# Kernel tuning notes

Measured on AMD Instinct MI355X. Metric: run time of the kernel, lower is better.

## Reference

```python
import jax, jax.numpy as jnp
import numpy as np

N_ENT = 100000
K = 64
D = 500            # emb_dim (complex half-dim); entity embedding is 2*D
R = 237            # num_relations
ATTN = 128
B = 1024
ETA_MAX = 0.5


def setup_inputs() -> dict:
    key = jax.random.key(0)
    ks = jax.random.split(key, 12)
    anchor_ids = jax.random.randint(ks[0], (B,), 0, N_ENT)
    nbr_ent = jax.random.randint(ks[1], (N_ENT, K), 0, N_ENT)
    nbr_rel = jax.random.randint(ks[2], (N_ENT, K), 0, R)
    nbr_dir = jax.random.randint(ks[3], (N_ENT, K), 0, 2).astype(bool)
    nbr_mask = jax.random.randint(ks[4], (N_ENT, K), 0, 2).astype(bool)
    freq = jax.random.uniform(ks[5], (N_ENT,), dtype=jnp.float32) * 1000.0
    entity_embedding = jax.random.normal(ks[6], (N_ENT, 2 * D), dtype=jnp.float32) * 0.1
    # relation phases; get_relation_reim -> (cos(phase), sin(phase))
    rel_phase = jax.random.uniform(ks[7], (R, D), dtype=jnp.float32, minval=-np.pi, maxval=np.pi)
    a_param = jnp.ones((D,), dtype=jnp.float32)
    eta_raw = jnp.float32(-6.0)
    w_raw = jnp.float32(1.0)
    b = jnp.float32(0.0)
    Wq = jax.random.normal(ks[8], (ATTN, 2 * D), dtype=jnp.float32) * 0.01
    Wk = jax.random.normal(ks[9], (ATTN, 2 * D), dtype=jnp.float32) * 0.01
    rel_bias = jax.random.normal(ks[10], (R, 1), dtype=jnp.float32) * 0.01
    dir_bias = jax.random.normal(ks[11], (2, 1), dtype=jnp.float32) * 0.01
    return dict(anchor_ids=anchor_ids, nbr_ent=nbr_ent, nbr_rel=nbr_rel,
                nbr_dir=nbr_dir, nbr_mask=nbr_mask, freq=freq,
                entity_embedding=entity_embedding, rel_phase=rel_phase,
                a_param=a_param, eta_raw=eta_raw, w_raw=w_raw, b=b,
                Wq=Wq, Wk=Wk, rel_bias=rel_bias, dir_bias=dir_bias)


def reference(anchor_ids, nbr_ent, nbr_rel, nbr_dir, nbr_mask, freq,
              entity_embedding, rel_phase, a_param, eta_raw, w_raw, b,
              Wq, Wk, rel_bias, dir_bias):
    # gather per-anchor neighbor tables: [B, K]
    a_ent = nbr_ent[anchor_ids]
    a_rel = nbr_rel[anchor_ids]
    a_dir = nbr_dir[anchor_ids]
    a_msk = nbr_mask[anchor_ids]

    # neighbor entity embeddings [B, K, 2D] -> complex halves [B, K, D]
    e_j = entity_embedding[a_ent]
    re_j, im_j = jnp.split(e_j, 2, axis=-1)

    # RotatE relation rotation (conjugate when dir==True)
    phase = rel_phase[a_rel]                      # [B, K, D]
    re_r = jnp.cos(phase)
    im_r = jnp.sin(phase)
    im_sel = jnp.where(a_dir[..., None], -im_r, im_r)
    re_msg = re_j * re_r - im_j * im_sel
    im_msg = re_j * im_sel + im_j * re_r
    hat = jnp.concatenate([re_msg, im_msg], axis=-1)  # [B, K, 2D]

    e_i = entity_embedding[anchor_ids]            # [B, 2D]

    # small QK attention with relation/direction bias
    q = e_i @ Wq.T                                # [B, A]
    k = hat @ Wk.T                                # [B, K, A]
    scale = max(ATTN ** 0.5, 1e-6)
    logits = jnp.einsum('ba,bka->bk', q, k) / scale
    dir_id = a_dir.astype(jnp.int32)
    logits = logits + rel_bias[a_rel][..., 0] + dir_bias[dir_id][..., 0]
    logits = jnp.where(a_msk, logits, -10000.0)

    has_nbr = jnp.any(a_msk, axis=1)              # [B]
    logits = jnp.where(has_nbr[:, None], logits, 0.0)
    attn = jax.nn.softmax(logits, axis=1)
    attn = jnp.where(has_nbr[:, None], attn, 0.0)

    delta = jnp.einsum('bk,bkd->bd', attn, hat)   # [B, 2D]
    delta = jnp.where(has_nbr[:, None], delta, e_i)

    # frequency-gated interpolation
    logf = jnp.log1p(freq[anchor_ids])
    w = jax.nn.softplus(w_raw)
    eta = ETA_MAX * jax.nn.sigmoid(eta_raw + w * (-logf) + b)
    eta = eta * has_nbr.astype(eta.dtype)

    re_d, im_d = jnp.split(delta, 2, axis=-1)
    re_d = a_param * re_d
    im_d = a_param * im_d
    re_i, im_i = jnp.split(e_i, 2, axis=-1)
    re_out = re_i + eta[:, None] * (re_d - re_i)
    im_out = im_i + eta[:, None] * (im_d - im_i)
    return jnp.concatenate([re_out, im_out], axis=-1)
```

## Files before the change

kernel.cpp:

```cpp
#include <hip/hip_runtime.h>
#include <math.h>

#define N_ENT 100000
#define KNBR 64
#define DHALF 500
#define TWO_D 1000
#define ATTN_DIM 128
#define ETA_MAX 0.5f

__global__ __launch_bounds__(256) void precompute_m(
    const int* __restrict__ anchor_ids,
    const float* __restrict__ E,
    const float* __restrict__ Wq,
    const float* __restrict__ Wk,
    float* __restrict__ M, int B)
{
    __shared__ float e_lds[8][TWO_D];
    __shared__ float qp[2][8][ATTN_DIM];
    __shared__ float q_lds[8][ATTN_DIM];
    const int t  = threadIdx.x;
    const int b0 = blockIdx.x * 8;

    for (int j = 0; j < 8; ++j) {
        int bb = b0 + j;
        int row = (bb < B) ? anchor_ids[bb] : 0;
        if (t < 250) {
            const float4* src = (const float4*)(E + (size_t)row * TWO_D);
            float4 v = src[t];
            e_lds[j][4 * t + 0] = v.x;
            e_lds[j][4 * t + 1] = v.y;
            e_lds[j][4 * t + 2] = v.z;
            e_lds[j][4 * t + 3] = v.w;
        }
    }
    __syncthreads();

    {
        const int a = t & 127;
        const int h = t >> 7;
        float acc[8] = {0.f, 0.f, 0.f, 0.f, 0.f, 0.f, 0.f, 0.f};
        const float* wrow = Wq + (size_t)a * TWO_D + h * DHALF;
        for (int d = 0; d < DHALF; ++d) {
            float w = wrow[d];
            int dd = h * DHALF + d;
#pragma unroll
            for (int j = 0; j < 8; ++j) acc[j] += w * e_lds[j][dd];
        }
#pragma unroll
        for (int j = 0; j < 8; ++j) qp[h][j][a] = acc[j];
    }
    __syncthreads();
    for (int idx = t; idx < 8 * ATTN_DIM; idx += 256) {
        ((float*)q_lds)[idx] = ((float*)qp)[idx] + ((float*)qp)[8 * ATTN_DIM + idx];
    }
    __syncthreads();

    const float inv_scale = 0.0883883476483184f;
    float acc2[4][8];
#pragma unroll
    for (int c = 0; c < 4; ++c)
#pragma unroll
        for (int j = 0; j < 8; ++j) acc2[c][j] = 0.f;

    for (int a = 0; a < ATTN_DIM; ++a) {
        const float* wkrow = Wk + (size_t)a * TWO_D;
        float wk[4];
#pragma unroll
        for (int c = 0; c < 4; ++c) {
            int d = t + 256 * c;
            wk[c] = (d < TWO_D) ? wkrow[d] : 0.f;
        }
#pragma unroll
        for (int j = 0; j < 8; ++j) {
            float qv = q_lds[j][a];
#pragma unroll
            for (int c = 0; c < 4; ++c) acc2[c][j] += qv * wk[c];
        }
    }
#pragma unroll
    for (int c = 0; c < 4; ++c) {
        int d = t + 256 * c;
        if (d < TWO_D) {
#pragma unroll
            for (int j = 0; j < 8; ++j) {
                int bb = b0 + j;
                if (bb < B) M[(size_t)bb * TWO_D + d] = acc2[c][j] * inv_scale;
            }
        }
    }
}

__global__ __launch_bounds__(256) void refine(
    const int* __restrict__ anchor_ids,
    const int* __restrict__ nbr_ent,
    const int* __restrict__ nbr_rel,
    const int* __restrict__ nbr_dir,
    const int* __restrict__ nbr_mask,
    const float* __restrict__ freq,
    const float* __restrict__ E,
    const float* __restrict__ P,
    const float* __restrict__ a_param,
    const float* __restrict__ eta_raw_p,
    const float* __restrict__ w_raw_p,
    const float* __restrict__ b_p,
    const float* __restrict__ rel_bias,
    const float* __restrict__ dir_bias,
    const float* __restrict__ M,
    float* __restrict__ out)
{
    __shared__ float m_lds[TWO_D];
    __shared__ float accm[4][TWO_D];
    __shared__ float sum_s[4];
    __shared__ int ent_s[KNBR], rel_s[KNBR], dir_s[KNBR], msk_s[KNBR];

    const int t = threadIdx.x;
    const int bid = blockIdx.x;
    const int anchor = anchor_ids[bid];

    for (int idx = t; idx < TWO_D; idx += 256)
        m_lds[idx] = M[(size_t)bid * TWO_D + idx];
    if (t < KNBR) {
        size_t off = (size_t)anchor * KNBR + t;
        ent_s[t] = nbr_ent[off];
        rel_s[t] = nbr_rel[off];
        dir_s[t] = nbr_dir[off];
        msk_s[t] = nbr_mask[off];
    }
    __syncthreads();

    const int lane = t & 63;
    const int wid = t >> 6;

    float mre[8], mim[8];
#pragma unroll
    for (int i = 0; i < 8; ++i) {
        int d = lane + 64 * i;
        mre[i] = (d < DHALF) ? m_lds[d] : 0.f;
        mim[i] = (d < DHALF) ? m_lds[DHALF + d] : 0.f;
    }

    float accre[8], accim[8];
#pragma unroll
    for (int i = 0; i < 8; ++i) { accre[i] = 0.f; accim[i] = 0.f; }
    float wsum = 0.f;
    const float db0 = dir_bias[0];
    const float db1 = dir_bias[1];

    for (int k = wid; k < KNBR; k += 4) {
        if (!msk_s[k]) continue;
        const int ent = ent_s[k];
        const int rel = rel_s[k];
        const int dirf = dir_s[k];
        const float* erow = E + (size_t)ent * TWO_D;
        const float* prow = P + (size_t)rel * DHALF;

        float hre[8], him[8];
        float dot = 0.f;
#pragma unroll
        for (int i = 0; i < 8; ++i) {
            int d = lane + 64 * i;
            if (d < DHALF) {
                float re = erow[d];
                float im = erow[DHALF + d];
                float ph = prow[d];
                float s, c;
                __sincosf(ph, &s, &c);
                if (dirf) s = -s;
                hre[i] = re * c - im * s;
                him[i] = re * s + im * c;
                dot += mre[i] * hre[i] + mim[i] * him[i];
            } else {
                hre[i] = 0.f;
                him[i] = 0.f;
            }
        }
        dot += __shfl_xor(dot, 32);
        dot += __shfl_xor(dot, 16);
        dot += __shfl_xor(dot, 8);
        dot += __shfl_xor(dot, 4);
        dot += __shfl_xor(dot, 2);
        dot += __shfl_xor(dot, 1);

        float logit = dot + rel_bias[rel] + (dirf ? db1 : db0);
        float p = __expf(logit);
        wsum += p;
#pragma unroll
        for (int i = 0; i < 8; ++i) {
            accre[i] += p * hre[i];
            accim[i] += p * him[i];
        }
    }

    if (lane == 0) sum_s[wid] = wsum;
#pragma unroll
    for (int i = 0; i < 8; ++i) {
        int d = lane + 64 * i;
        if (d < DHALF) {
            accm[wid][d] = accre[i];
            accm[wid][DHALF + d] = accim[i];
        }
    }
    __syncthreads();

    const float S = sum_s[0] + sum_s[1] + sum_s[2] + sum_s[3];
    const float invS = (S > 0.f) ? 1.f / S : 0.f;
    float eta = 0.f;
    if (S > 0.f) {
        float logf_ = log1pf(freq[anchor]);
        float wv = log1pf(__expf(w_raw_p[0]));
        float x = eta_raw_p[0] - wv * logf_ + b_p[0];
        eta = ETA_MAX / (1.f + __expf(-x));
    }

    const float* eirow = E + (size_t)anchor * TWO_D;
#pragma unroll
    for (int c = 0; c < 4; ++c) {
        int dd = t + 256 * c;
        if (dd < TWO_D) {
            float delta = (accm[0][dd] + accm[1][dd] + accm[2][dd] + accm[3][dd]) * invS;
            float ei = eirow[dd];
            float ap = a_param[(dd < DHALF) ? dd : dd - DHALF];
            out[(size_t)bid * TWO_D + dd] = ei + eta * (ap * delta - ei);
        }
    }
}

extern "C" void kernel_launch(void* const* d_in, const int* in_sizes, int n_in,
                              void* d_out, int out_size, void* d_ws, size_t ws_size,
                              hipStream_t stream)
{
    const int*   anchor_ids = (const int*)d_in[0];
    const int*   nbr_ent    = (const int*)d_in[1];
    const int*   nbr_rel    = (const int*)d_in[2];
    const int*   nbr_dir    = (const int*)d_in[3];
    const int*   nbr_mask   = (const int*)d_in[4];
    const float* freq       = (const float*)d_in[5];
    const float* E          = (const float*)d_in[6];
    const float* P          = (const float*)d_in[7];
    const float* a_param    = (const float*)d_in[8];
    const float* eta_raw    = (const float*)d_in[9];
    const float* w_raw      = (const float*)d_in[10];
    const float* b_scalar   = (const float*)d_in[11];
    const float* Wq         = (const float*)d_in[12];
    const float* Wk         = (const float*)d_in[13];
    const float* rel_bias   = (const float*)d_in[14];
    const float* dir_bias   = (const float*)d_in[15];
    float* out = (float*)d_out;

    const int B = in_sizes[0];
    float* M = (float*)d_ws;

    precompute_m<<<(B + 7) / 8, 256, 0, stream>>>(anchor_ids, E, Wq, Wk, M, B);
    refine<<<B, 256, 0, stream>>>(anchor_ids, nbr_ent, nbr_rel, nbr_dir, nbr_mask,
                                  freq, E, P, a_param, eta_raw, w_raw, b_scalar,
                                  rel_bias, dir_bias, M, out);
}
```

Baseline: 629.1 us.

## Precompute Wq^T Wk, sincos tables, tiled M GEMM, and compacted prefetching neighbor loop

Replaces the per-anchor Q/K projection with a precomputed 1000x1000 matrix G2 = Wq^T Wk / scale, followed by a tiled GEMM from gathered anchor embeddings to M. Relation cos/sin values now come from tables built once per call instead of per-neighbor sincos. The refine kernel compacts masked neighbors with a ballot, folds the relation and direction biases in up front, and software-prefetches the next neighbor's float4 rows while computing the current one. In exchange it adds more kernel launches and a larger GEMM (1000x1000x128 plus 1024x1000x1000), which may cost more FLOPs than the original factored path.

```diff
diff --git a/kernel.cpp b/kernel.cpp
--- a/kernel.cpp
+++ b/kernel.cpp
@@ -1,93 +1,189 @@
 #include <hip/hip_runtime.h>
 #include <math.h>
 
-#define N_ENT 100000
 #define KNBR 64
 #define DHALF 500
 #define TWO_D 1000
 #define ATTN_DIM 128
 #define ETA_MAX 0.5f
 
-__global__ __launch_bounds__(256) void precompute_m(
-    const int* __restrict__ anchor_ids,
-    const float* __restrict__ E,
-    const float* __restrict__ Wq,
-    const float* __restrict__ Wk,
-    float* __restrict__ M, int B)
-{
-    __shared__ float e_lds[8][TWO_D];
-    __shared__ float qp[2][8][ATTN_DIM];
-    __shared__ float q_lds[8][ATTN_DIM];
-    const int t  = threadIdx.x;
-    const int b0 = blockIdx.x * 8;
-
-    for (int j = 0; j < 8; ++j) {
-        int bb = b0 + j;
-        int row = (bb < B) ? anchor_ids[bb] : 0;
-        if (t < 250) {
-            const float4* src = (const float4*)(E + (size_t)row * TWO_D);
-            float4 v = src[t];
-            e_lds[j][4 * t + 0] = v.x;
-            e_lds[j][4 * t + 1] = v.y;
-            e_lds[j][4 * t + 2] = v.z;
-            e_lds[j][4 * t + 3] = v.w;
-        }
+__global__ __launch_bounds__(256) void build_tables(
+    const float* __restrict__ P, float* __restrict__ ctab,
+    float* __restrict__ stab, int R)
+{
+    int idx = blockIdx.x * 256 + threadIdx.x;
+    if (idx >= R * 512) return;
+    int r = idx >> 9, d = idx & 511;
+    float c = 0.f, s = 0.f;
+    if (d < DHALF) { float ph = P[r * DHALF + d]; sincosf(ph, &s, &c); }
+    ctab[idx] = c;
+    stab[idx] = s;
+}
+
+__global__ __launch_bounds__(256) void build_g2(
+    const float* __restrict__ Wq, const float* __restrict__ Wk,
+    float* __restrict__ G2)
+{
+    __shared__ float At[ATTN_DIM][64];
+    __shared__ float Bt[ATTN_DIM][64];
+    const int t = threadIdx.x;
+    const int d1_0 = blockIdx.y * 64, d2_0 = blockIdx.x * 64;
+#pragma unroll
+    for (int i = 0; i < 32; ++i) {
+        int idx = t + 256 * i;
+        int a = idx >> 6, c = idx & 63;
+        int d1 = d1_0 + c, d2 = d2_0 + c;
+        At[a][c] = (d1 < TWO_D) ? Wq[(size_t)a * TWO_D + d1] : 0.f;
+        Bt[a][c] = (d2 < TWO_D) ? Wk[(size_t)a * TWO_D + d2] : 0.f;
     }
     __syncthreads();
-
-    {
-        const int a = t & 127;
-        const int h = t >> 7;
-        float acc[8] = {0.f, 0.f, 0.f, 0.f, 0.f, 0.f, 0.f, 0.f};
-        const float* wrow = Wq + (size_t)a * TWO_D + h * DHALF;
-        for (int d = 0; d < DHALF; ++d) {
-            float w = wrow[d];
-            int dd = h * DHALF + d;
-#pragma unroll
-            for (int j = 0; j < 8; ++j) acc[j] += w * e_lds[j][dd];
-        }
-#pragma unroll
-        for (int j = 0; j < 8; ++j) qp[h][j][a] = acc[j];
-    }
+    const int tx = t & 15, ty = t >> 4;
+    float acc[4][4] = {};
+    for (int a = 0; a < ATTN_DIM; ++a) {
+        float av[4], bv[4];
+#pragma unroll
+        for (int i = 0; i < 4; ++i) av[i] = At[a][4 * ty + i];
+#pragma unroll
+        for (int j = 0; j < 4; ++j) bv[j] = Bt[a][4 * tx + j];
+#pragma unroll
+        for (int i = 0; i < 4; ++i)
+#pragma unroll
+            for (int j = 0; j < 4; ++j) acc[i][j] += av[i] * bv[j];
+    }
+    const float inv_scale = 0.0883883476483184f;
+#pragma unroll
+    for (int i = 0; i < 4; ++i) {
+        int d1 = d1_0 + 4 * ty + i;
+        if (d1 < TWO_D) {
+#pragma unroll
+            for (int j = 0; j < 4; ++j) {
+                int d2 = d2_0 + 4 * tx + j;
+                G2[(size_t)d1 * 1024 + d2] = acc[i][j] * inv_scale;
+            }
+        }
+    }
+}
+
+__global__ __launch_bounds__(256) void gemm_M(
+    const int* __restrict__ anchor_ids, const float* __restrict__ E,
+    const float* __restrict__ G2, float* __restrict__ M, int B)
+{
+    __shared__ float At[64][33];
+    __shared__ float Bt[32][64];
+    __shared__ int rows_s[64];
+    const int t = threadIdx.x;
+    const int bx = blockIdx.x, by = blockIdx.y;
+    if (t < 64) { int bb = by * 64 + t; rows_s[t] = (bb < B) ? anchor_ids[bb] : 0; }
     __syncthreads();
-    for (int idx = t; idx < 8 * ATTN_DIM; idx += 256) {
-        ((float*)q_lds)[idx] = ((float*)qp)[idx] + ((float*)qp)[8 * ATTN_DIM + idx];
-    }
-    __syncthreads();
-
-    const float inv_scale = 0.0883883476483184f;
-    float acc2[4][8];
-#pragma unroll
-    for (int c = 0; c < 4; ++c)
-#pragma unroll
-        for (int j = 0; j < 8; ++j) acc2[c][j] = 0.f;
-
-    for (int a = 0; a < ATTN_DIM; ++a) {
-        const float* wkrow = Wk + (size_t)a * TWO_D;
-        float wk[4];
-#pragma unroll
-        for (int c = 0; c < 4; ++c) {
-            int d = t + 256 * c;
-            wk[c] = (d < TWO_D) ? wkrow[d] : 0.f;
-        }
-#pragma unroll
-        for (int j = 0; j < 8; ++j) {
-            float qv = q_lds[j][a];
-#pragma unroll
-            for (int c = 0; c < 4; ++c) acc2[c][j] += qv * wk[c];
-        }
-    }
-#pragma unroll
-    for (int c = 0; c < 4; ++c) {
-        int d = t + 256 * c;
-        if (d < TWO_D) {
-#pragma unroll
-            for (int j = 0; j < 8; ++j) {
-                int bb = b0 + j;
-                if (bb < B) M[(size_t)bb * TWO_D + d] = acc2[c][j] * inv_scale;
+    const int tx = t & 15, ty = t >> 4;
+    float acc[4][4] = {};
+    for (int k0 = 0; k0 < TWO_D; k0 += 32) {
+#pragma unroll
+        for (int i = 0; i < 8; ++i) {
+            int idx = t + 256 * i;
+            int r = idx >> 5, c = idx & 31;
+            int k = k0 + c;
+            At[r][c] = (k < TWO_D) ? E[(size_t)rows_s[r] * TWO_D + k] : 0.f;
+        }
+#pragma unroll
+        for (int i = 0; i < 8; ++i) {
+            int idx = t + 256 * i;
+            int r = idx >> 6, c = idx & 63;
+            int k = k0 + r;
+            Bt[r][c] = (k < TWO_D) ? G2[(size_t)k * 1024 + bx * 64 + c] : 0.f;
+        }
+        __syncthreads();
+#pragma unroll
+        for (int kk = 0; kk < 32; ++kk) {
+            float av[4], bv[4];
+#pragma unroll
+            for (int i = 0; i < 4; ++i) av[i] = At[4 * ty + i][kk];
+#pragma unroll
+            for (int j = 0; j < 4; ++j) bv[j] = Bt[kk][4 * tx + j];
+#pragma unroll
+            for (int i = 0; i < 4; ++i)
+#pragma unroll
+                for (int j = 0; j < 4; ++j) acc[i][j] += av[i] * bv[j];
+        }
+        __syncthreads();
+    }
+#pragma unroll
+    for (int i = 0; i < 4; ++i) {
+        int b = by * 64 + 4 * ty + i;
+        if (b < B) {
+#pragma unroll
+            for (int j = 0; j < 4; ++j) {
+                int d2 = bx * 64 + 4 * tx + j;
+                if (d2 < TWO_D) M[(size_t)b * TWO_D + d2] = acc[i][j];
             }
         }
     }
+}
+
+struct NbrData {
+    float4 re0, re1, im0, im1, c0, c1, s0, s1;
+    float rb, ds;
+};
+
+__device__ __forceinline__ void load_nbr(
+    int j, int lane, const float* __restrict__ E,
+    const float* __restrict__ ctab, const float* __restrict__ stab,
+    const int* ent_s, const int* rel_s, const float* rb_s, const float* ds_s,
+    NbrData& n)
+{
+    const int ent = ent_s[j];
+    const int rel = rel_s[j];
+    const float4* er = (const float4*)(E + (size_t)ent * TWO_D);
+    const float4* cr = (const float4*)(ctab + (size_t)rel * 512);
+    const float4* sr = (const float4*)(stab + (size_t)rel * 512);
+    n.re0 = er[lane];
+    n.im0 = er[125 + lane];
+    n.re1 = make_float4(0.f, 0.f, 0.f, 0.f);
+    n.im1 = make_float4(0.f, 0.f, 0.f, 0.f);
+    if (lane < 61) {
+        n.re1 = er[64 + lane];
+        n.im1 = er[189 + lane];
+    }
+    n.c0 = cr[lane];      n.c1 = cr[64 + lane];
+    n.s0 = sr[lane];      n.s1 = sr[64 + lane];
+    n.rb = rb_s[j];
+    n.ds = ds_s[j];
+}
+
+__device__ __forceinline__ void compute_nbr(
+    const NbrData& n,
+    const float4& mre0, const float4& mre1, const float4& mim0, const float4& mim1,
+    float4& are0, float4& are1, float4& aim0, float4& aim1, float& wsum)
+{
+    const float ds = n.ds;
+    float4 hre0, hre1, him0, him1;
+    float dot = 0.f;
+#define ROT_DOT(F)                                                              \
+    {                                                                           \
+        float se0 = n.s0.F * ds;                                                \
+        hre0.F = n.re0.F * n.c0.F - n.im0.F * se0;                              \
+        him0.F = n.re0.F * se0 + n.im0.F * n.c0.F;                              \
+        dot += mre0.F * hre0.F + mim0.F * him0.F;                               \
+        float se1 = n.s1.F * ds;                                                \
+        hre1.F = n.re1.F * n.c1.F - n.im1.F * se1;                              \
+        him1.F = n.re1.F * se1 + n.im1.F * n.c1.F;                              \
+        dot += mre1.F * hre1.F + mim1.F * him1.F;                               \
+    }
+    ROT_DOT(x) ROT_DOT(y) ROT_DOT(z) ROT_DOT(w)
+#undef ROT_DOT
+    dot += __shfl_xor(dot, 32);
+    dot += __shfl_xor(dot, 16);
+    dot += __shfl_xor(dot, 8);
+    dot += __shfl_xor(dot, 4);
+    dot += __shfl_xor(dot, 2);
+    dot += __shfl_xor(dot, 1);
+    const float p = __expf(dot + n.rb);
+    wsum += p;
+#define ACC(F)                                                                  \
+    are0.F += p * hre0.F; are1.F += p * hre1.F;                                 \
+    aim0.F += p * him0.F; aim1.F += p * him1.F;
+    ACC(x) ACC(y) ACC(z) ACC(w)
+#undef ACC
 }
 
 __global__ __launch_bounds__(256) void refine(
@@ -98,7 +194,8 @@
     const int* __restrict__ nbr_mask,
     const float* __restrict__ freq,
     const float* __restrict__ E,
-    const float* __restrict__ P,
+    const float* __restrict__ ctab,
+    const float* __restrict__ stab,
     const float* __restrict__ a_param,
     const float* __restrict__ eta_raw_p,
     const float* __restrict__ w_raw_p,
@@ -108,97 +205,66 @@
     const float* __restrict__ M,
     float* __restrict__ out)
 {
-    __shared__ float m_lds[TWO_D];
     __shared__ float accm[4][TWO_D];
     __shared__ float sum_s[4];
-    __shared__ int ent_s[KNBR], rel_s[KNBR], dir_s[KNBR], msk_s[KNBR];
+    __shared__ int ent_s[KNBR], rel_s[KNBR];
+    __shared__ float rb_s[KNBR], ds_s[KNBR];
+    __shared__ int act_n_s;
 
     const int t = threadIdx.x;
     const int bid = blockIdx.x;
-    const int anchor = anchor_ids[bid];
-
-    for (int idx = t; idx < TWO_D; idx += 256)
-        m_lds[idx] = M[(size_t)bid * TWO_D + idx];
-    if (t < KNBR) {
-        size_t off = (size_t)anchor * KNBR + t;
-        ent_s[t] = nbr_ent[off];
-        rel_s[t] = nbr_rel[off];
-        dir_s[t] = nbr_dir[off];
-        msk_s[t] = nbr_mask[off];
-    }
-    __syncthreads();
-
     const int lane = t & 63;
     const int wid = t >> 6;
-
-    float mre[8], mim[8];
-#pragma unroll
-    for (int i = 0; i < 8; ++i) {
-        int d = lane + 64 * i;
-        mre[i] = (d < DHALF) ? m_lds[d] : 0.f;
-        mim[i] = (d < DHALF) ? m_lds[DHALF + d] : 0.f;
-    }
-
-    float accre[8], accim[8];
-#pragma unroll
-    for (int i = 0; i < 8; ++i) { accre[i] = 0.f; accim[i] = 0.f; }
+    const int anchor = anchor_ids[bid];
+
+    if (wid == 0) {
+        size_t off = (size_t)anchor * KNBR + lane;
+        int msk = nbr_mask[off];
+        unsigned long long bal = __ballot(msk != 0);
+        if (msk) {
+            int rank = __popcll(bal & ((1ull << lane) - 1ull));
+            int rel = nbr_rel[off];
+            int dirf = nbr_dir[off];
+            ent_s[rank] = nbr_ent[off];
+            rel_s[rank] = rel;
+            ds_s[rank] = dirf ? -1.f : 1.f;
+            rb_s[rank] = rel_bias[rel] + dir_bias[dirf ? 1 : 0];
+        }
+        if (lane == 0) act_n_s = (int)__popcll(bal);
+    }
+    __syncthreads();
+    const int an = act_n_s;
+
+    const float4* mr = (const float4*)(M + (size_t)bid * TWO_D);
+    float4 mre0 = mr[lane];
+    float4 mim0 = mr[125 + lane];
+    float4 mre1 = make_float4(0.f, 0.f, 0.f, 0.f);
+    float4 mim1 = make_float4(0.f, 0.f, 0.f, 0.f);
+    if (lane < 61) { mre1 = mr[64 + lane]; mim1 = mr[189 + lane]; }
+
+    float4 are0 = make_float4(0.f, 0.f, 0.f, 0.f), are1 = are0, aim0 = are0, aim1 = are0;
     float wsum = 0.f;
-    const float db0 = dir_bias[0];
-    const float db1 = dir_bias[1];
-
-    for (int k = wid; k < KNBR; k += 4) {
-        if (!msk_s[k]) continue;
-        const int ent = ent_s[k];
-        const int rel = rel_s[k];
-        const int dirf = dir_s[k];
-        const float* erow = E + (size_t)ent * TWO_D;
-        const float* prow = P + (size_t)rel * DHALF;
-
-        float hre[8], him[8];
-        float dot = 0.f;
-#pragma unroll
-        for (int i = 0; i < 8; ++i) {
-            int d = lane + 64 * i;
-            if (d < DHALF) {
-                float re = erow[d];
-                float im = erow[DHALF + d];
-                float ph = prow[d];
-                float s, c;
-                __sincosf(ph, &s, &c);
-                if (dirf) s = -s;
-                hre[i] = re * c - im * s;
-                him[i] = re * s + im * c;
-                dot += mre[i] * hre[i] + mim[i] * him[i];
-            } else {
-                hre[i] = 0.f;
-                him[i] = 0.f;
-            }
-        }
-        dot += __shfl_xor(dot, 32);
-        dot += __shfl_xor(dot, 16);
-        dot += __shfl_xor(dot, 8);
-        dot += __shfl_xor(dot, 4);
-        dot += __shfl_xor(dot, 2);
-        dot += __shfl_xor(dot, 1);
-
-        float logit = dot + rel_bias[rel] + (dirf ? db1 : db0);
-        float p = __expf(logit);
-        wsum += p;
-#pragma unroll
-        for (int i = 0; i < 8; ++i) {
-            accre[i] += p * hre[i];
-            accim[i] += p * him[i];
-        }
+
+    NbrData cur, nxt;
+    int j = wid;
+    bool have = (j < an);
+    if (have) load_nbr(j, lane, E, ctab, stab, ent_s, rel_s, rb_s, ds_s, cur);
+    while (have) {
+        int jn = j + 4;
+        bool haveN = (jn < an);
+        if (haveN) load_nbr(jn, lane, E, ctab, stab, ent_s, rel_s, rb_s, ds_s, nxt);
+        compute_nbr(cur, mre0, mre1, mim0, mim1, are0, are1, aim0, aim1, wsum);
+        cur = nxt;
+        j = jn;
+        have = haveN;
     }
 
     if (lane == 0) sum_s[wid] = wsum;
-#pragma unroll
-    for (int i = 0; i < 8; ++i) {
-        int d = lane + 64 * i;
-        if (d < DHALF) {
-            accm[wid][d] = accre[i];
-            accm[wid][DHALF + d] = accim[i];
-        }
+    {
+        float4* am = (float4*)(&accm[wid][0]);
+        am[lane] = are0;
+        am[125 + lane] = aim0;
+        if (lane < 61) { am[64 + lane] = are1; am[189 + lane] = aim1; }
     }
     __syncthreads();
 
@@ -248,10 +314,23 @@
     float* out = (float*)d_out;
 
     const int B = in_sizes[0];
-    float* M = (float*)d_ws;
-
-    precompute_m<<<(B + 7) / 8, 256, 0, stream>>>(anchor_ids, E, Wq, Wk, M, B);
+    const int R = in_sizes[7] / DHALF;
+
+    auto align256 = [](size_t x) { return (x + 255) & ~(size_t)255; };
+    char* ws = (char*)d_ws;
+    size_t offM  = 0;
+    size_t offG2 = align256(offM + (size_t)B * TWO_D * 4);
+    size_t offC  = align256(offG2 + (size_t)TWO_D * 1024 * 4);
+    size_t offS  = align256(offC + (size_t)R * 512 * 4);
+    float* M    = (float*)(ws + offM);
+    float* G2   = (float*)(ws + offG2);
+    float* ctab = (float*)(ws + offC);
+    float* stab = (float*)(ws + offS);
+
+    build_tables<<<(R * 512 + 255) / 256, 256, 0, stream>>>(P, ctab, stab, R);
+    build_g2<<<dim3(16, 16), 256, 0, stream>>>(Wq, Wk, G2);
+    gemm_M<<<dim3(16, (B + 63) / 64), 256, 0, stream>>>(anchor_ids, E, G2, M, B);
     refine<<<B, 256, 0, stream>>>(anchor_ids, nbr_ent, nbr_rel, nbr_dir, nbr_mask,
-                                  freq, E, P, a_param, eta_raw, w_raw, b_scalar,
-                                  rel_bias, dir_bias, M, out);
-}
+                                  freq, E, ctab, stab, a_param, eta_raw, w_raw,
+                                  b_scalar, rel_bias, dir_bias, M, out);
+}
```

After: 733.3 us. 16.6% more time.
